# Kernel tuning notes

Measured on AMD Instinct MI355X. Metric: run time of the kernel, lower is better.

## Reference

```python
import jax, jax.numpy as jnp
import numpy as np

POI_LEN = 38333
FEAT = 898
EMBED = 128
OUT_DIM = 128
K = 1  # masked entries per node (mask has exactly K True per row)
E = POI_LEN * 32


def _glorot(key, shape):
    fan_in = shape[0]
    return jax.random.normal(key, shape, jnp.float32) / np.float32(np.sqrt(fan_in))


def setup_inputs() -> dict:
    key = jax.random.key(0)
    ks = jax.random.split(key, 16)
    x = jax.random.normal(ks[0], (POI_LEN, FEAT), jnp.float32)
    # column 0 holds POI ids (as floats), selected by the mask
    ids = jax.random.randint(ks[1], (POI_LEN,), 0, POI_LEN, jnp.int32)
    x = x.at[:, 0].set(ids.astype(jnp.float32))
    mask = jnp.zeros((POI_LEN, FEAT), jnp.bool_).at[:, 0].set(True)
    edge_index = jax.random.randint(ks[2], (2, E), 0, POI_LEN, jnp.int32)
    return {
        "x": x,
        "edge_index": edge_index,
        "mask": mask,
        "emb": jax.random.normal(ks[3], (POI_LEN, EMBED), jnp.float32),
        "W1": _glorot(ks[4], (FEAT, 64)), "b1": jnp.zeros((64,), jnp.float32),
        "W2": _glorot(ks[5], (64, 32)), "b2": jnp.zeros((32,), jnp.float32),
        "W3": _glorot(ks[6], (32, 32)), "b3": jnp.zeros((32,), jnp.float32),
        "W4": _glorot(ks[7], (32, 32)), "b4": jnp.zeros((32,), jnp.float32),
        "W5": _glorot(ks[8], (32, 1)), "b5": jnp.zeros((1,), jnp.float32),
        "fcW1": _glorot(ks[9], (POI_LEN, 128)), "fcb1": jnp.zeros((128,), jnp.float32),
        "fcW2": _glorot(ks[10], (128, OUT_DIM)), "fcb2": jnp.zeros((OUT_DIM,), jnp.float32),
    }


def reference(x, edge_index, mask, emb, W1, b1, W2, b2, W3, b3, W4, b4, W5, b5,
              fcW1, fcb1, fcW2, fcb2):
    N, F = x.shape
    # --- masked_select -> poi ids; embedding; masked_scatter back ---
    mask_flat = mask.reshape(-1)
    # stable argsort puts True positions first, in row-major order
    order = jnp.argsort(jnp.logical_not(mask_flat), stable=True)
    M = N * K  # number of True entries (static)
    sel = order[:M]
    poi = x.reshape(-1)[sel].astype(jnp.int32)       # [M] poi ids
    emb_poi = emb[poi.reshape(N, K)]                  # [N, K, EMBED]
    # masked_scatter: fill the M True slots with the first M source elements
    feat = x.reshape(-1).at[sel].set(emb_poi.reshape(-1)[:M]).reshape(N, F)
    # --- GCN normalization with self-loops (PyG GCNConv default) ---
    loops = jnp.arange(N, dtype=edge_index.dtype)
    src = jnp.concatenate([edge_index[0], loops])
    dst = jnp.concatenate([edge_index[1], loops])
    deg = jax.ops.segment_sum(jnp.ones(src.shape, feat.dtype), dst, num_segments=N)
    dis = jnp.where(deg > 0, jax.lax.rsqrt(jnp.maximum(deg, 1.0)), 0.0)
    norm = (dis[src] * dis[dst])[:, None]             # [E+N, 1]

    def gcn(h, W, b):
        h = h @ W                                     # [N, out]
        agg = jax.ops.segment_sum(h[src] * norm, dst, num_segments=N)
        return agg + b

    lrelu = lambda v: jax.nn.leaky_relu(v, 0.01)
    h = lrelu(gcn(feat, W1, b1))
    h = lrelu(gcn(h, W2, b2))
    t = gcn(h, W3, b3)
    h = lrelu(t) + t
    t = gcn(h, W4, b4)
    h = lrelu(t) + t
    h = lrelu(gcn(h, W5, b5)).reshape(-1)             # [N]
    out = jax.nn.relu(h @ fcW1 + fcb1)
    out = jax.nn.relu(out @ fcW2 + fcb2)              # [OUT_DIM]
    return out
```

## Files before the change

kernel.cpp:

```cpp
#include <hip/hip_runtime.h>
#include <math.h>

#define NPOI 38333
#define FEATD 898
#define EMBD 128
#define KPAD 928
#define NKT 29
#define SPLIT0 15

typedef short s16x8 __attribute__((ext_vector_type(8)));
typedef float f32x4 __attribute__((ext_vector_type(4)));

__global__ __launch_bounds__(256) void init_kernel(const float* __restrict__ x,
                                                   const float* __restrict__ emb,
                                                   float* __restrict__ c0,
                                                   int* __restrict__ cnt) {
  int i = blockIdx.x * 256 + threadIdx.x;
  if (i < NPOI) {
    int id = (int)x[(size_t)(i >> 7) * FEATD];
    c0[i] = emb[(size_t)id * EMBD + (i & 127)];
    cnt[i] = 0;
  }
}

__global__ __launch_bounds__(256) void hist_kernel(const int* __restrict__ dst,
                                                   int* __restrict__ cnt, int E) {
  int e = blockIdx.x * 256 + threadIdx.x;
  if (e < E) atomicAdd(&cnt[dst[e]], 1);
}

__global__ __launch_bounds__(256) void dis_kernel(const int* __restrict__ cnt,
                                                  float* __restrict__ dis) {
  int i = blockIdx.x * 256 + threadIdx.x;
  if (i < NPOI) dis[i] = 1.0f / sqrtf((float)(cnt[i] + 1));
}

__global__ __launch_bounds__(256) void wsplit_kernel(const float* __restrict__ W1,
                                                     unsigned short* __restrict__ WhiT,
                                                     unsigned short* __restrict__ WloT) {
  int n = blockIdx.x;
  for (int k = threadIdx.x; k < KPAD; k += 256) {
    float f = (k < FEATD) ? W1[(size_t)k * 64 + n] : 0.0f;
    unsigned b = __float_as_uint(f);
    unsigned hb = b & 0xFFFF0000u;
    float r = f - __uint_as_float(hb);
    unsigned rb = __float_as_uint(r) & 0xFFFF0000u;
    WhiT[(size_t)n * KPAD + k] = (unsigned short)(hb >> 16);
    WloT[(size_t)n * KPAD + k] = (unsigned short)(rb >> 16);
  }
}

__global__ __launch_bounds__(1024) void scan_kernel(const int* __restrict__ cnt,
                                                    int* __restrict__ rs,
                                                    int* __restrict__ cur) {
  const int t = threadIdx.x;
  const int CH = (NPOI + 1023) >> 10;
  int lo = t * CH, hi = lo + CH;
  if (lo > NPOI) lo = NPOI;
  if (hi > NPOI) hi = NPOI;
  int s = 0;
  for (int i = lo; i < hi; ++i) s += cnt[i];
  const int lane = t & 63, wid = t >> 6;
  int v = s;
#pragma unroll
  for (int d = 1; d < 64; d <<= 1) {
    int u = __shfl_up(v, d, 64);
    if (lane >= d) v += u;
  }
  __shared__ int wsum[16];
  __shared__ int woff[17];
  if (lane == 63) wsum[wid] = v;
  __syncthreads();
  if (t == 0) {
    int run = 0;
    for (int i = 0; i < 16; ++i) { woff[i] = run; run += wsum[i]; }
    woff[16] = run;
  }
  __syncthreads();
  int run = woff[wid] + v - s;
  for (int i = lo; i < hi; ++i) {
    rs[i] = run;
    cur[i] = 0;
    run += cnt[i];
  }
  if (t == 1023) rs[NPOI] = woff[16];
}

__global__ __launch_bounds__(256) void fill_kernel(const int* __restrict__ src,
                                                   const int* __restrict__ dst,
                                                   const float* __restrict__ dis,
                                                   const int* __restrict__ rs,
                                                   int* __restrict__ cur,
                                                   int* __restrict__ neigh,
                                                   float* __restrict__ nw, int E) {
  int e = blockIdx.x * 256 + threadIdx.x;
  if (e >= E) return;
  int d = dst[e], s = src[e];
  int pos = rs[d] + atomicAdd(&cur[d], 1);
  neigh[pos] = s;
  nw[pos] = dis[s];
}

__global__ __launch_bounds__(512) void gemm1_mfma(const float* __restrict__ x,
                                                  const float* __restrict__ c0,
                                                  const unsigned short* __restrict__ WhiT,
                                                  const unsigned short* __restrict__ WloT,
                                                  float* __restrict__ out) {
  __shared__ unsigned short smem[2][4][64][40];

  const int tid = threadIdx.x;
  const int half = tid >> 8;
  const int t = tid & 255;
  const int row0 = blockIdx.x * 64;
  const int wv = (tid >> 6) & 3;
  const int lane = tid & 63;
  const int m16 = lane & 15, kg = lane >> 4;

  f32x4 acc[4] = {};

  const int kt0 = half ? SPLIT0 : 0;
  const int kt1 = half ? NKT : SPLIT0;

  for (int it = 0; it < SPLIT0; ++it) {
    const int kt = kt0 + it;
    const bool active = kt < kt1;
    if (active) {
      const int k0 = kt * 32;
#pragma unroll
      for (int i = 0; i < 4; ++i) {
        int fid = t + i * 256;
        int row = fid >> 4, kq2 = fid & 15;
        int k = k0 + kq2 * 2;
        float2 v = {0.0f, 0.0f};
        int grow = row0 + row;
        if (grow < NPOI && k < FEATD) {
          v = *(const float2*)&x[(size_t)grow * FEATD + k];
          if (k == 0) v.x = c0[grow];
        }
        unsigned b0 = __float_as_uint(v.x), b1 = __float_as_uint(v.y);
        unsigned h0 = b0 & 0xFFFF0000u, h1 = b1 & 0xFFFF0000u;
        float r0 = v.x - __uint_as_float(h0);
        float r1 = v.y - __uint_as_float(h1);
        unsigned l0 = __float_as_uint(r0) & 0xFFFF0000u;
        unsigned l1 = __float_as_uint(r1) & 0xFFFF0000u;
        *(unsigned*)&smem[half][0][row][kq2 * 2] = (h0 >> 16) | h1;
        *(unsigned*)&smem[half][1][row][kq2 * 2] = (l0 >> 16) | l1;
      }
#pragma unroll
      for (int i = 0; i < 2; ++i) {
        int fid = t + i * 256;
        int col = fid >> 3, kq = fid & 7;
        int k = kt * 32 + kq * 4;
        *(uint2*)&smem[half][2][col][kq * 4] =
            *(const uint2*)&WhiT[(size_t)col * KPAD + k];
        *(uint2*)&smem[half][3][col][kq * 4] =
            *(const uint2*)&WloT[(size_t)col * KPAD + k];
      }
    }
    __syncthreads();
    if (active) {
      s16x8 a_hi = *(const s16x8*)&smem[half][0][wv * 16 + m16][kg * 8];
      s16x8 a_lo = *(const s16x8*)&smem[half][1][wv * 16 + m16][kg * 8];
#pragma unroll
      for (int g = 0; g < 4; ++g) {
        s16x8 b_hi = *(const s16x8*)&smem[half][2][g * 16 + m16][kg * 8];
        s16x8 b_lo = *(const s16x8*)&smem[half][3][g * 16 + m16][kg * 8];
        acc[g] = __builtin_amdgcn_mfma_f32_16x16x32_bf16(a_hi, b_hi, acc[g], 0, 0, 0);
        acc[g] = __builtin_amdgcn_mfma_f32_16x16x32_bf16(a_hi, b_lo, acc[g], 0, 0, 0);
        acc[g] = __builtin_amdgcn_mfma_f32_16x16x32_bf16(a_lo, b_hi, acc[g], 0, 0, 0);
      }
    }
    __syncthreads();
  }

  float (*red)[64] = (float(*)[64])smem;
  if (half == 1) {
#pragma unroll
    for (int g = 0; g < 4; ++g)
#pragma unroll
      for (int r = 0; r < 4; ++r)
        red[wv * 16 + kg * 4 + r][g * 16 + m16] = acc[g][r];
  }
  __syncthreads();
  if (half == 0) {
#pragma unroll
    for (int g = 0; g < 4; ++g)
#pragma unroll
      for (int r = 0; r < 4; ++r) {
        int grow = row0 + wv * 16 + kg * 4 + r;
        if (grow < NPOI)
          out[(size_t)grow * 64 + g * 16 + m16] =
              acc[g][r] + red[wv * 16 + kg * 4 + r][g * 16 + m16];
      }
  }
}

template <int ACT>
__global__ __launch_bounds__(256) void gather64_kernel(const float* __restrict__ hw,
                                                       const float* __restrict__ dis,
                                                       const int* __restrict__ rs,
                                                       const int* __restrict__ neigh,
                                                       const float* __restrict__ nw,
                                                       const float* __restrict__ b,
                                                       float* __restrict__ out) {
  int node = blockIdx.x * 4 + (threadIdx.x >> 6);
  if (node >= NPOI) return;
  int f = threadIdx.x & 63;
  float dd = dis[node];
  float acc = dd * hw[(size_t)node * 64 + f];
  int j = rs[node];
  const int j1 = rs[node + 1];
  for (; j + 7 < j1; j += 8) {
    int s0 = neigh[j], s1 = neigh[j + 1], s2 = neigh[j + 2], s3 = neigh[j + 3];
    int s4 = neigh[j + 4], s5 = neigh[j + 5], s6 = neigh[j + 6], s7 = neigh[j + 7];
    float w0 = nw[j], w1 = nw[j + 1], w2 = nw[j + 2], w3 = nw[j + 3];
    float w4 = nw[j + 4], w5 = nw[j + 5], w6 = nw[j + 6], w7 = nw[j + 7];
    acc += w0 * hw[(size_t)s0 * 64 + f];
    acc += w1 * hw[(size_t)s1 * 64 + f];
    acc += w2 * hw[(size_t)s2 * 64 + f];
    acc += w3 * hw[(size_t)s3 * 64 + f];
    acc += w4 * hw[(size_t)s4 * 64 + f];
    acc += w5 * hw[(size_t)s5 * 64 + f];
    acc += w6 * hw[(size_t)s6 * 64 + f];
    acc += w7 * hw[(size_t)s7 * 64 + f];
  }
  for (; j < j1; ++j) acc += nw[j] * hw[(size_t)neigh[j] * 64 + f];
  float v = dd * acc + b[f];
  float l = v > 0.0f ? v : 0.01f * v;
  out[(size_t)node * 64 + f] = ACT ? (l + v) : l;
}

template <int ACT>
__global__ __launch_bounds__(256) void gather32_kernel(const float* __restrict__ hw,
                                                       const float* __restrict__ dis,
                                                       const int* __restrict__ rs,
                                                       const int* __restrict__ neigh,
                                                       const float* __restrict__ nw,
                                                       const float* __restrict__ b,
                                                       float* __restrict__ out) {
  int node = blockIdx.x * 8 + (threadIdx.x >> 5);
  if (node >= NPOI) return;
  int f = threadIdx.x & 31;
  float dd = dis[node];
  float acc = dd * hw[(size_t)node * 32 + f];
  int j = rs[node];
  const int j1 = rs[node + 1];
  for (; j + 7 < j1; j += 8) {
    int s0 = neigh[j], s1 = neigh[j + 1], s2 = neigh[j + 2], s3 = neigh[j + 3];
    int s4 = neigh[j + 4], s5 = neigh[j + 5], s6 = neigh[j + 6], s7 = neigh[j + 7];
    float w0 = nw[j], w1 = nw[j + 1], w2 = nw[j + 2], w3 = nw[j + 3];
    float w4 = nw[j + 4], w5 = nw[j + 5], w6 = nw[j + 6], w7 = nw[j + 7];
    acc += w0 * hw[(size_t)s0 * 32 + f];
    acc += w1 * hw[(size_t)s1 * 32 + f];
    acc += w2 * hw[(size_t)s2 * 32 + f];
    acc += w3 * hw[(size_t)s3 * 32 + f];
    acc += w4 * hw[(size_t)s4 * 32 + f];
    acc += w5 * hw[(size_t)s5 * 32 + f];
    acc += w6 * hw[(size_t)s6 * 32 + f];
    acc += w7 * hw[(size_t)s7 * 32 + f];
  }
  for (; j < j1; ++j) acc += nw[j] * hw[(size_t)neigh[j] * 32 + f];
  float v = dd * acc + b[f];
  float l = v > 0.0f ? v : 0.01f * v;
  out[(size_t)node * 32 + f] = ACT ? (l + v) : l;
}

__global__ __launch_bounds__(256) void gather1_kernel(const float* __restrict__ h5w,
                                                      const float* __restrict__ dis,
                                                      const int* __restrict__ rs,
                                                      const int* __restrict__ neigh,
                                                      const float* __restrict__ nw,
                                                      const float* __restrict__ b5,
                                                      float* __restrict__ out) {
  int node = blockIdx.x * 4 + (threadIdx.x >> 6);
  if (node >= NPOI) return;
  int lane = threadIdx.x & 63;
  float dd = dis[node];
  float acc = 0.0f;
  const int j0 = rs[node], j1 = rs[node + 1];
  for (int j = j0 + lane; j < j1; j += 64) acc += nw[j] * h5w[neigh[j]];
#pragma unroll
  for (int d = 32; d > 0; d >>= 1) acc += __shfl_down(acc, d, 64);
  if (lane == 0) {
    float v = dd * (acc + dd * h5w[node]) + b5[0];
    out[node] = v > 0.0f ? v : 0.01f * v;
  }
}

template <int KIN>
__global__ __launch_bounds__(256) void gemm_small32(const float* __restrict__ h,
                                                    const float* __restrict__ W,
                                                    float* __restrict__ out) {
  __shared__ float Ws[KIN * 32];
  __shared__ float Hs[8][KIN];
  const int tid = threadIdx.x;
  const int row0 = blockIdx.x * 8;
  for (int l = tid; l < KIN * 32; l += 256) Ws[l] = W[l];
  for (int l = tid; l < 8 * KIN; l += 256) {
    int r = l / KIN, k = l % KIN;
    int row = row0 + r;
    Hs[r][k] = (row < NPOI) ? h[(size_t)row * KIN + k] : 0.0f;
  }
  __syncthreads();
  const int r = tid >> 5, c = tid & 31;
  float acc = 0.0f;
#pragma unroll
  for (int k = 0; k < KIN; ++k) acc += Hs[r][k] * Ws[k * 32 + c];
  int row = row0 + r;
  if (row < NPOI) out[(size_t)row * 32 + c] = acc;
}

__global__ __launch_bounds__(256) void gemm_w5(const float* __restrict__ h,
                                               const float* __restrict__ W5,
                                               float* __restrict__ out) {
  __shared__ float Ws[32];
  if (threadIdx.x < 32) Ws[threadIdx.x] = W5[threadIdx.x];
  __syncthreads();
  int i = blockIdx.x * 256 + threadIdx.x;
  if (i >= NPOI) return;
  float acc = 0.0f;
#pragma unroll
  for (int k = 0; k < 32; ++k) acc += h[(size_t)i * 32 + k] * Ws[k];
  out[i] = acc;
}

__global__ __launch_bounds__(128) void matvec_kernel(const float* __restrict__ h5,
                                                     const float* __restrict__ fcW1,
                                                     float* __restrict__ part) {
  int j = threadIdx.x;
  int b = blockIdx.x;
  int i0 = b * 64, iend = i0 + 64;
  if (iend > NPOI) iend = NPOI;
  float a0 = 0.0f, a1 = 0.0f, a2 = 0.0f, a3 = 0.0f;
  int i = i0;
  for (; i + 3 < iend; i += 4) {
    a0 += h5[i + 0] * fcW1[(size_t)(i + 0) * 128 + j];
    a1 += h5[i + 1] * fcW1[(size_t)(i + 1) * 128 + j];
    a2 += h5[i + 2] * fcW1[(size_t)(i + 2) * 128 + j];
    a3 += h5[i + 3] * fcW1[(size_t)(i + 3) * 128 + j];
  }
  for (; i < iend; ++i) a0 += h5[i] * fcW1[(size_t)i * 128 + j];
  part[(size_t)b * 128 + j] = (a0 + a1) + (a2 + a3);
}

__global__ __launch_bounds__(64) void reduce_kernel(const float* __restrict__ part,
                                                    int npart,
                                                    const float* __restrict__ fcb1,
                                                    float* __restrict__ h1) {
  const int j = blockIdx.x;
  const int lane = threadIdx.x;
  float acc = 0.0f;
  for (int b = lane; b < npart; b += 64) acc += part[(size_t)b * 128 + j];
#pragma unroll
  for (int d = 32; d > 0; d >>= 1) acc += __shfl_down(acc, d, 64);
  if (lane == 0) {
    float v = acc + fcb1[j];
    h1[j] = v > 0.0f ? v : 0.0f;
  }
}

__global__ __launch_bounds__(64) void head2_kernel(const float* __restrict__ h1,
                                                   const float* __restrict__ fcW2,
                                                   const float* __restrict__ fcb2,
                                                   float* __restrict__ out) {
  const int t = blockIdx.x;
  const int lane = threadIdx.x;
  float acc = h1[lane] * fcW2[(size_t)lane * 128 + t] +
              h1[lane + 64] * fcW2[(size_t)(lane + 64) * 128 + t];
#pragma unroll
  for (int d = 32; d > 0; d >>= 1) acc += __shfl_down(acc, d, 64);
  if (lane == 0) {
    float v = acc + fcb2[t];
    out[t] = v > 0.0f ? v : 0.0f;
  }
}

extern "C" void kernel_launch(void* const* d_in, const int* in_sizes, int n_in,
                              void* d_out, int out_size, void* d_ws, size_t ws_size,
                              hipStream_t stream) {
  const float* x    = (const float*)d_in[0];
  const int*   ei   = (const int*)d_in[1];
  const float* emb  = (const float*)d_in[3];
  const float* W1   = (const float*)d_in[4];
  const float* b1   = (const float*)d_in[5];
  const float* W2   = (const float*)d_in[6];
  const float* b2   = (const float*)d_in[7];
  const float* W3   = (const float*)d_in[8];
  const float* b3   = (const float*)d_in[9];
  const float* W4   = (const float*)d_in[10];
  const float* b4   = (const float*)d_in[11];
  const float* W5   = (const float*)d_in[12];
  const float* b5   = (const float*)d_in[13];
  const float* fcW1 = (const float*)d_in[14];
  const float* fcb1 = (const float*)d_in[15];
  const float* fcW2 = (const float*)d_in[16];
  const float* fcb2 = (const float*)d_in[17];
  float* out = (float*)d_out;

  const int E = in_sizes[1] / 2;
  const int* srcE = ei;
  const int* dstE = ei + E;

  float* ws = (float*)d_ws;
  size_t off = 0;
  auto carve = [&](size_t n) {
    float* p = ws + off;
    off += (n + 255) & ~(size_t)255;
    return p;
  };
  float* c0    = carve(NPOI);
  float* dis   = carve(NPOI);
  int*   cnt   = (int*)carve(NPOI);
  int*   rs    = (int*)carve(NPOI + 1);
  int*   cur   = (int*)carve(NPOI);
  int*   neigh = (int*)carve(E);
  float* nw    = carve(E);
  unsigned short* WhiT = (unsigned short*)carve(64 * KPAD / 2);
  unsigned short* WloT = (unsigned short*)carve(64 * KPAD / 2);
  float* p0    = carve((size_t)NPOI * 64);
  float* bufH  = carve((size_t)NPOI * 64);
  const int NMV = (NPOI + 63) / 64;
  float* part  = carve((size_t)NMV * 128);
  float* h1    = carve(128);
  (void)ws_size; (void)n_in; (void)out_size;

  const int gN    = (NPOI + 255) / 256;
  const int gE    = (E + 255) / 256;
  const int gG64  = (NPOI + 3) / 4;
  const int gG32  = (NPOI + 7) / 8;
  const int gS    = (NPOI + 7) / 8;
  const int GB1   = (NPOI + 63) / 64;

  init_kernel<<<gN, 256, 0, stream>>>(x, emb, c0, cnt);
  hist_kernel<<<gE, 256, 0, stream>>>(dstE, cnt, E);
  scan_kernel<<<1, 1024, 0, stream>>>(cnt, rs, cur);
  dis_kernel<<<gN, 256, 0, stream>>>(cnt, dis);
  fill_kernel<<<gE, 256, 0, stream>>>(srcE, dstE, dis, rs, cur, neigh, nw, E);
  wsplit_kernel<<<64, 256, 0, stream>>>(W1, WhiT, WloT);

  gemm1_mfma<<<GB1, 512, 0, stream>>>(x, c0, WhiT, WloT, p0);
  gather64_kernel<0><<<gG64, 256, 0, stream>>>(p0, dis, rs, neigh, nw, b1, bufH);

  gemm_small32<64><<<gS, 256, 0, stream>>>(bufH, W2, p0);
  gather32_kernel<0><<<gG32, 256, 0, stream>>>(p0, dis, rs, neigh, nw, b2, bufH);

  gemm_small32<32><<<gS, 256, 0, stream>>>(bufH, W3, p0);
  gather32_kernel<1><<<gG32, 256, 0, stream>>>(p0, dis, rs, neigh, nw, b3, bufH);

  gemm_small32<32><<<gS, 256, 0, stream>>>(bufH, W4, p0);
  gather32_kernel<1><<<gG32, 256, 0, stream>>>(p0, dis, rs, neigh, nw, b4, bufH);

  gemm_w5<<<gN, 256, 0, stream>>>(bufH, W5, p0);
  gather1_kernel<<<gG64, 256, 0, stream>>>(p0, dis, rs, neigh, nw, b5, c0);

  matvec_kernel<<<NMV, 128, 0, stream>>>(c0, fcW1, part);
  reduce_kernel<<<128, 64, 0, stream>>>(part, NMV, fcb1, h1);
  head2_kernel<<<128, 64, 0, stream>>>(h1, fcW2, fcb2, out);
}
```

Measured before the change: 733.8 us.

## Fold source normalization into GEMM outputs, compress neighbor list to u16, drop LDS in gemm1

Result: no change. 726.1 us (-1.1%).

```diff
diff --git a/kernel.cpp b/kernel.cpp
--- a/kernel.cpp
+++ b/kernel.cpp
@@ -88,109 +88,101 @@
 
 __global__ __launch_bounds__(256) void fill_kernel(const int* __restrict__ src,
                                                    const int* __restrict__ dst,
-                                                   const float* __restrict__ dis,
                                                    const int* __restrict__ rs,
                                                    int* __restrict__ cur,
-                                                   int* __restrict__ neigh,
-                                                   float* __restrict__ nw, int E) {
+                                                   unsigned short* __restrict__ neigh,
+                                                   int E) {
   int e = blockIdx.x * 256 + threadIdx.x;
   if (e >= E) return;
   int d = dst[e], s = src[e];
   int pos = rs[d] + atomicAdd(&cur[d], 1);
-  neigh[pos] = s;
-  nw[pos] = dis[s];
-}
-
-__global__ __launch_bounds__(512) void gemm1_mfma(const float* __restrict__ x,
+  neigh[pos] = (unsigned short)s;
+}
+
+__global__ __launch_bounds__(256) void gemm1_mfma(const float* __restrict__ x,
                                                   const float* __restrict__ c0,
                                                   const unsigned short* __restrict__ WhiT,
                                                   const unsigned short* __restrict__ WloT,
+                                                  const float* __restrict__ dis,
                                                   float* __restrict__ out) {
-  __shared__ unsigned short smem[2][4][64][40];
+  __shared__ float red[64][65];
 
   const int tid = threadIdx.x;
-  const int half = tid >> 8;
-  const int t = tid & 255;
-  const int row0 = blockIdx.x * 64;
-  const int wv = (tid >> 6) & 3;
-  const int lane = tid & 63;
-  const int m16 = lane & 15, kg = lane >> 4;
-
-  f32x4 acc[4] = {};
-
-  const int kt0 = half ? SPLIT0 : 0;
-  const int kt1 = half ? NKT : SPLIT0;
-
-  for (int it = 0; it < SPLIT0; ++it) {
-    const int kt = kt0 + it;
-    const bool active = kt < kt1;
-    if (active) {
-      const int k0 = kt * 32;
-#pragma unroll
-      for (int i = 0; i < 4; ++i) {
-        int fid = t + i * 256;
-        int row = fid >> 4, kq2 = fid & 15;
-        int k = k0 + kq2 * 2;
+  const int wv = tid >> 6, lane = tid & 63;
+  const int kh = wv & 1, rh = wv >> 1;
+  const int m16 = lane & 15, kq = lane >> 4;
+  const int row0 = blockIdx.x * 64 + rh * 32;
+
+  f32x4 acc[2][4] = {};
+  const int t0 = kh ? SPLIT0 : 0;
+  const int t1 = kh ? NKT : SPLIT0;
+
+  for (int kt = t0; kt < t1; ++kt) {
+    const int kbase = kt * 32 + kq * 8;
+    s16x8 bh[4], bl[4];
+#pragma unroll
+    for (int g = 0; g < 4; ++g) {
+      const size_t cb = (size_t)(g * 16 + m16) * KPAD + kbase;
+      bh[g] = *(const s16x8*)&WhiT[cb];
+      bl[g] = *(const s16x8*)&WloT[cb];
+    }
+#pragma unroll
+    for (int m = 0; m < 2; ++m) {
+      const int row = row0 + m * 16 + m16;
+      const bool rok = row < NPOI;
+      float f[8];
+#pragma unroll
+      for (int q = 0; q < 4; ++q) {
+        const int k = kbase + q * 2;
         float2 v = {0.0f, 0.0f};
-        int grow = row0 + row;
-        if (grow < NPOI && k < FEATD) {
-          v = *(const float2*)&x[(size_t)grow * FEATD + k];
-          if (k == 0) v.x = c0[grow];
-        }
-        unsigned b0 = __float_as_uint(v.x), b1 = __float_as_uint(v.y);
-        unsigned h0 = b0 & 0xFFFF0000u, h1 = b1 & 0xFFFF0000u;
-        float r0 = v.x - __uint_as_float(h0);
-        float r1 = v.y - __uint_as_float(h1);
-        unsigned l0 = __float_as_uint(r0) & 0xFFFF0000u;
-        unsigned l1 = __float_as_uint(r1) & 0xFFFF0000u;
-        *(unsigned*)&smem[half][0][row][kq2 * 2] = (h0 >> 16) | h1;
-        *(unsigned*)&smem[half][1][row][kq2 * 2] = (l0 >> 16) | l1;
+        if (rok && k < FEATD) v = *(const float2*)&x[(size_t)row * FEATD + k];
+        f[q * 2] = v.x;
+        f[q * 2 + 1] = v.y;
       }
-#pragma unroll
-      for (int i = 0; i < 2; ++i) {
-        int fid = t + i * 256;
-        int col = fid >> 3, kq = fid & 7;
-        int k = kt * 32 + kq * 4;
-        *(uint2*)&smem[half][2][col][kq * 4] =
-            *(const uint2*)&WhiT[(size_t)col * KPAD + k];
-        *(uint2*)&smem[half][3][col][kq * 4] =
-            *(const uint2*)&WloT[(size_t)col * KPAD + k];
+      if (kbase == 0 && rok) f[0] = c0[row];
+      s16x8 ah, al;
+#pragma unroll
+      for (int j = 0; j < 8; ++j) {
+        unsigned b = __float_as_uint(f[j]);
+        unsigned hb = b & 0xFFFF0000u;
+        float r = f[j] - __uint_as_float(hb);
+        unsigned lb = __float_as_uint(r) & 0xFFFF0000u;
+        ah[j] = (short)(hb >> 16);
+        al[j] = (short)(lb >> 16);
+      }
+#pragma unroll
+      for (int g = 0; g < 4; ++g) {
+        acc[m][g] = __builtin_amdgcn_mfma_f32_16x16x32_bf16(ah, bh[g], acc[m][g], 0, 0, 0);
+        acc[m][g] = __builtin_amdgcn_mfma_f32_16x16x32_bf16(ah, bl[g], acc[m][g], 0, 0, 0);
+        acc[m][g] = __builtin_amdgcn_mfma_f32_16x16x32_bf16(al, bh[g], acc[m][g], 0, 0, 0);
       }
     }
-    __syncthreads();
-    if (active) {
-      s16x8 a_hi = *(const s16x8*)&smem[half][0][wv * 16 + m16][kg * 8];
-      s16x8 a_lo = *(const s16x8*)&smem[half][1][wv * 16 + m16][kg * 8];
-#pragma unroll
-      for (int g = 0; g < 4; ++g) {
-        s16x8 b_hi = *(const s16x8*)&smem[half][2][g * 16 + m16][kg * 8];
-        s16x8 b_lo = *(const s16x8*)&smem[half][3][g * 16 + m16][kg * 8];
-        acc[g] = __builtin_amdgcn_mfma_f32_16x16x32_bf16(a_hi, b_hi, acc[g], 0, 0, 0);
-        acc[g] = __builtin_amdgcn_mfma_f32_16x16x32_bf16(a_hi, b_lo, acc[g], 0, 0, 0);
-        acc[g] = __builtin_amdgcn_mfma_f32_16x16x32_bf16(a_lo, b_hi, acc[g], 0, 0, 0);
-      }
-    }
-    __syncthreads();
-  }
-
-  float (*red)[64] = (float(*)[64])smem;
-  if (half == 1) {
-#pragma unroll
-    for (int g = 0; g < 4; ++g)
-#pragma unroll
-      for (int r = 0; r < 4; ++r)
-        red[wv * 16 + kg * 4 + r][g * 16 + m16] = acc[g][r];
+  }
+
+  if (kh == 1) {
+#pragma unroll
+    for (int m = 0; m < 2; ++m)
+#pragma unroll
+      for (int g = 0; g < 4; ++g)
+#pragma unroll
+        for (int r = 0; r < 4; ++r)
+          red[rh * 32 + m * 16 + kq * 4 + r][g * 16 + m16] = acc[m][g][r];
   }
   __syncthreads();
-  if (half == 0) {
-#pragma unroll
-    for (int g = 0; g < 4; ++g)
+  if (kh == 0) {
+#pragma unroll
+    for (int m = 0; m < 2; ++m)
 #pragma unroll
       for (int r = 0; r < 4; ++r) {
-        int grow = row0 + wv * 16 + kg * 4 + r;
-        if (grow < NPOI)
-          out[(size_t)grow * 64 + g * 16 + m16] =
-              acc[g][r] + red[wv * 16 + kg * 4 + r][g * 16 + m16];
+        const int lrow = rh * 32 + m * 16 + kq * 4 + r;
+        const int grow = row0 + m * 16 + kq * 4 + r;
+        if (grow < NPOI) {
+          const float dd = dis[grow];
+#pragma unroll
+          for (int g = 0; g < 4; ++g)
+            out[(size_t)grow * 64 + g * 16 + m16] =
+                (acc[m][g][r] + red[lrow][g * 16 + m16]) * dd;
+        }
       }
   }
 }
@@ -199,32 +191,29 @@
 __global__ __launch_bounds__(256) void gather64_kernel(const float* __restrict__ hw,
                                                        const float* __restrict__ dis,
                                                        const int* __restrict__ rs,
-                                                       const int* __restrict__ neigh,
-                                                       const float* __restrict__ nw,
+                                                       const unsigned short* __restrict__ neigh,
                                                        const float* __restrict__ b,
                                                        float* __restrict__ out) {
   int node = blockIdx.x * 4 + (threadIdx.x >> 6);
   if (node >= NPOI) return;
   int f = threadIdx.x & 63;
   float dd = dis[node];
-  float acc = dd * hw[(size_t)node * 64 + f];
+  float acc = hw[(size_t)node * 64 + f];
   int j = rs[node];
   const int j1 = rs[node + 1];
   for (; j + 7 < j1; j += 8) {
     int s0 = neigh[j], s1 = neigh[j + 1], s2 = neigh[j + 2], s3 = neigh[j + 3];
     int s4 = neigh[j + 4], s5 = neigh[j + 5], s6 = neigh[j + 6], s7 = neigh[j + 7];
-    float w0 = nw[j], w1 = nw[j + 1], w2 = nw[j + 2], w3 = nw[j + 3];
-    float w4 = nw[j + 4], w5 = nw[j + 5], w6 = nw[j + 6], w7 = nw[j + 7];
-    acc += w0 * hw[(size_t)s0 * 64 + f];
-    acc += w1 * hw[(size_t)s1 * 64 + f];
-    acc += w2 * hw[(size_t)s2 * 64 + f];
-    acc += w3 * hw[(size_t)s3 * 64 + f];
-    acc += w4 * hw[(size_t)s4 * 64 + f];
-    acc += w5 * hw[(size_t)s5 * 64 + f];
-    acc += w6 * hw[(size_t)s6 * 64 + f];
-    acc += w7 * hw[(size_t)s7 * 64 + f];
-  }
-  for (; j < j1; ++j) acc += nw[j] * hw[(size_t)neigh[j] * 64 + f];
+    acc += hw[(size_t)s0 * 64 + f];
+    acc += hw[(size_t)s1 * 64 + f];
+    acc += hw[(size_t)s2 * 64 + f];
+    acc += hw[(size_t)s3 * 64 + f];
+    acc += hw[(size_t)s4 * 64 + f];
+    acc += hw[(size_t)s5 * 64 + f];
+    acc += hw[(size_t)s6 * 64 + f];
+    acc += hw[(size_t)s7 * 64 + f];
+  }
+  for (; j < j1; ++j) acc += hw[(size_t)neigh[j] * 64 + f];
   float v = dd * acc + b[f];
   float l = v > 0.0f ? v : 0.01f * v;
   out[(size_t)node * 64 + f] = ACT ? (l + v) : l;
@@ -234,32 +223,29 @@
 __global__ __launch_bounds__(256) void gather32_kernel(const float* __restrict__ hw,
                                                        const float* __restrict__ dis,
                                                        const int* __restrict__ rs,
-                                                       const int* __restrict__ neigh,
-                                                       const float* __restrict__ nw,
+                                                       const unsigned short* __restrict__ neigh,
                                                        const float* __restrict__ b,
                                                        float* __restrict__ out) {
   int node = blockIdx.x * 8 + (threadIdx.x >> 5);
   if (node >= NPOI) return;
   int f = threadIdx.x & 31;
   float dd = dis[node];
-  float acc = dd * hw[(size_t)node * 32 + f];
+  float acc = hw[(size_t)node * 32 + f];
   int j = rs[node];
   const int j1 = rs[node + 1];
   for (; j + 7 < j1; j += 8) {
     int s0 = neigh[j], s1 = neigh[j + 1], s2 = neigh[j + 2], s3 = neigh[j + 3];
     int s4 = neigh[j + 4], s5 = neigh[j + 5], s6 = neigh[j + 6], s7 = neigh[j + 7];
-    float w0 = nw[j], w1 = nw[j + 1], w2 = nw[j + 2], w3 = nw[j + 3];
-    float w4 = nw[j + 4], w5 = nw[j + 5], w6 = nw[j + 6], w7 = nw[j + 7];
-    acc += w0 * hw[(size_t)s0 * 32 + f];
-    acc += w1 * hw[(size_t)s1 * 32 + f];
-    acc += w2 * hw[(size_t)s2 * 32 + f];
-    acc += w3 * hw[(size_t)s3 * 32 + f];
-    acc += w4 * hw[(size_t)s4 * 32 + f];
-    acc += w5 * hw[(size_t)s5 * 32 + f];
-    acc += w6 * hw[(size_t)s6 * 32 + f];
-    acc += w7 * hw[(size_t)s7 * 32 + f];
-  }
-  for (; j < j1; ++j) acc += nw[j] * hw[(size_t)neigh[j] * 32 + f];
+    acc += hw[(size_t)s0 * 32 + f];
+    acc += hw[(size_t)s1 * 32 + f];
+    acc += hw[(size_t)s2 * 32 + f];
+    acc += hw[(size_t)s3 * 32 + f];
+    acc += hw[(size_t)s4 * 32 + f];
+    acc += hw[(size_t)s5 * 32 + f];
+    acc += hw[(size_t)s6 * 32 + f];
+    acc += hw[(size_t)s7 * 32 + f];
+  }
+  for (; j < j1; ++j) acc += hw[(size_t)neigh[j] * 32 + f];
   float v = dd * acc + b[f];
   float l = v > 0.0f ? v : 0.01f * v;
   out[(size_t)node * 32 + f] = ACT ? (l + v) : l;
@@ -268,8 +254,7 @@
 __global__ __launch_bounds__(256) void gather1_kernel(const float* __restrict__ h5w,
                                                       const float* __restrict__ dis,
                                                       const int* __restrict__ rs,
-                                                      const int* __restrict__ neigh,
-                                                      const float* __restrict__ nw,
+                                                      const unsigned short* __restrict__ neigh,
                                                       const float* __restrict__ b5,
                                                       float* __restrict__ out) {
   int node = blockIdx.x * 4 + (threadIdx.x >> 6);
@@ -278,11 +263,11 @@
   float dd = dis[node];
   float acc = 0.0f;
   const int j0 = rs[node], j1 = rs[node + 1];
-  for (int j = j0 + lane; j < j1; j += 64) acc += nw[j] * h5w[neigh[j]];
+  for (int j = j0 + lane; j < j1; j += 64) acc += h5w[neigh[j]];
 #pragma unroll
   for (int d = 32; d > 0; d >>= 1) acc += __shfl_down(acc, d, 64);
   if (lane == 0) {
-    float v = dd * (acc + dd * h5w[node]) + b5[0];
+    float v = dd * (acc + h5w[node]) + b5[0];
     out[node] = v > 0.0f ? v : 0.01f * v;
   }
 }
@@ -290,6 +275,7 @@
 template <int KIN>
 __global__ __launch_bounds__(256) void gemm_small32(const float* __restrict__ h,
                                                     const float* __restrict__ W,
+                                                    const float* __restrict__ dis,
                                                     float* __restrict__ out) {
   __shared__ float Ws[KIN * 32];
   __shared__ float Hs[8][KIN];
@@ -307,11 +293,12 @@
 #pragma unroll
   for (int k = 0; k < KIN; ++k) acc += Hs[r][k] * Ws[k * 32 + c];
   int row = row0 + r;
-  if (row < NPOI) out[(size_t)row * 32 + c] = acc;
+  if (row < NPOI) out[(size_t)row * 32 + c] = acc * dis[row];
 }
 
 __global__ __launch_bounds__(256) void gemm_w5(const float* __restrict__ h,
                                                const float* __restrict__ W5,
+                                               const float* __restrict__ dis,
                                                float* __restrict__ out) {
   __shared__ float Ws[32];
   if (threadIdx.x < 32) Ws[threadIdx.x] = W5[threadIdx.x];
@@ -321,7 +308,7 @@
   float acc = 0.0f;
 #pragma unroll
   for (int k = 0; k < 32; ++k) acc += h[(size_t)i * 32 + k] * Ws[k];
-  out[i] = acc;
+  out[i] = acc * dis[i];
 }
 
 __global__ __launch_bounds__(128) void matvec_kernel(const float* __restrict__ h5,
@@ -413,10 +400,9 @@
   int*   cnt   = (int*)carve(NPOI);
   int*   rs    = (int*)carve(NPOI + 1);
   int*   cur   = (int*)carve(NPOI);
-  int*   neigh = (int*)carve(E);
-  float* nw    = carve(E);
-  unsigned short* WhiT = (unsigned short*)carve(64 * KPAD / 2);
-  unsigned short* WloT = (unsigned short*)carve(64 * KPAD / 2);
+  unsigned short* neigh = (unsigned short*)carve((E + 1) / 2);
+  unsigned short* WhiT  = (unsigned short*)carve(64 * KPAD / 2);
+  unsigned short* WloT  = (unsigned short*)carve(64 * KPAD / 2);
   float* p0    = carve((size_t)NPOI * 64);
   float* bufH  = carve((size_t)NPOI * 64);
   const int NMV = (NPOI + 63) / 64;
@@ -435,23 +421,23 @@
   hist_kernel<<<gE, 256, 0, stream>>>(dstE, cnt, E);
   scan_kernel<<<1, 1024, 0, stream>>>(cnt, rs, cur);
   dis_kernel<<<gN, 256, 0, stream>>>(cnt, dis);
-  fill_kernel<<<gE, 256, 0, stream>>>(srcE, dstE, dis, rs, cur, neigh, nw, E);
+  fill_kernel<<<gE, 256, 0, stream>>>(srcE, dstE, rs, cur, neigh, E);
   wsplit_kernel<<<64, 256, 0, stream>>>(W1, WhiT, WloT);
 
-  gemm1_mfma<<<GB1, 512, 0, stream>>>(x, c0, WhiT, WloT, p0);
-  gather64_kernel<0><<<gG64, 256, 0, stream>>>(p0, dis, rs, neigh, nw, b1, bufH);
-
-  gemm_small32<64><<<gS, 256, 0, stream>>>(bufH, W2, p0);
-  gather32_kernel<0><<<gG32, 256, 0, stream>>>(p0, dis, rs, neigh, nw, b2, bufH);
-
-  gemm_small32<32><<<gS, 256, 0, stream>>>(bufH, W3, p0);
-  gather32_kernel<1><<<gG32, 256, 0, stream>>>(p0, dis, rs, neigh, nw, b3, bufH);
-
-  gemm_small32<32><<<gS, 256, 0, stream>>>(bufH, W4, p0);
-  gather32_kernel<1><<<gG32, 256, 0, stream>>>(p0, dis, rs, neigh, nw, b4, bufH);
-
-  gemm_w5<<<gN, 256, 0, stream>>>(bufH, W5, p0);
-  gather1_kernel<<<gG64, 256, 0, stream>>>(p0, dis, rs, neigh, nw, b5, c0);
+  gemm1_mfma<<<GB1, 256, 0, stream>>>(x, c0, WhiT, WloT, dis, p0);
+  gather64_kernel<0><<<gG64, 256, 0, stream>>>(p0, dis, rs, neigh, b1, bufH);
+
+  gemm_small32<64><<<gS, 256, 0, stream>>>(bufH, W2, dis, p0);
+  gather32_kernel<0><<<gG32, 256, 0, stream>>>(p0, dis, rs, neigh, b2, bufH);
+
+  gemm_small32<32><<<gS, 256, 0, stream>>>(bufH, W3, dis, p0);
+  gather32_kernel<1><<<gG32, 256, 0, stream>>>(p0, dis, rs, neigh, b3, bufH);
+
+  gemm_small32<32><<<gS, 256, 0, stream>>>(bufH, W4, dis, p0);
+  gather32_kernel<1><<<gG32, 256, 0, stream>>>(p0, dis, rs, neigh, b4, bufH);
+
+  gemm_w5<<<gN, 256, 0, stream>>>(bufH, W5, dis, p0);
+  gather1_kernel<<<gG64, 256, 0, stream>>>(p0, dis, rs, neigh, b5, c0);
 
   matvec_kernel<<<NMV, 128, 0, stream>>>(c0, fcW1, part);
   reduce_kernel<<<128, 64, 0, stream>>>(part, NMV, fcb1, h1);
```
